# Performance work log

Hardware: AMD Instinct MI355X
Metric: run time of the kernel (lower is better)

## Reference

```python
import jax, jax.numpy as jnp
import numpy as np

N_NODES = 100000
N_EDGES = 1600000
D = 64
N_LAYERS = 3


def setup_inputs() -> dict:
    key = jax.random.key(0)
    k1, k2, k3, k4 = jax.random.split(key, 4)
    x = jax.random.normal(k1, (N_NODES, D), dtype=jnp.float32)
    edge_index = jax.random.randint(k2, (2, N_EDGES), 0, N_NODES, dtype=jnp.int64)
    scale = 1.0 / np.sqrt(D)
    Wl = jax.random.normal(k3, (N_LAYERS, D, D), dtype=jnp.float32) * scale
    Wr = jax.random.normal(k4, (N_LAYERS, D, D), dtype=jnp.float32) * scale
    b = jnp.zeros((N_LAYERS, D), dtype=jnp.float32)
    return {"x": x, "edge_index": edge_index, "Wl": Wl, "Wr": Wr, "b": b}


def _sage_conv(x, src, dst, Wl, Wr, b, n_nodes):
    # mean-aggregate source features onto targets, then two linear maps
    msgs = x[src]                                              # [E, d]
    summed = jax.ops.segment_sum(msgs, dst, num_segments=n_nodes)   # [N, d]
    cnt = jax.ops.segment_sum(jnp.ones(src.shape[0], x.dtype), dst,
                              num_segments=n_nodes)            # [N]
    agg = summed / jnp.maximum(cnt, 1.0)[:, None]
    return agg @ Wl + x @ Wr + b


def reference(x, edge_index, Wl, Wr, b):
    # GraphSAGE forward in eval mode (dropout is identity, p=0.5 only in training)
    src, dst = edge_index[0], edge_index[1]
    n = x.shape[0]
    h = x
    for i in range(N_LAYERS - 1):
        h = _sage_conv(h, src, dst, Wl[i], Wr[i], b[i], n)
        h = jax.nn.relu(h)
    h = _sage_conv(h, src, dst, Wl[-1], Wr[-1], b[-1], n)
    return h
```

## Files before the change

kernel.cpp:

```cpp
#include <hip/hip_runtime.h>
#include <hip/hip_fp16.h>

#define DD 64
#define NPB 32
#define EPC 8192
#define BK_SHIFT 9
#define BNODES 512
#define SCHUNK 1024
#define APAD 136

typedef _Float16 half8 __attribute__((ext_vector_type(8)));
typedef float f32x4 __attribute__((ext_vector_type(4)));

union U8 { uint2 u; __half2 h[2]; };

__global__ __launch_bounds__(256) void prep_kernel(
    const float* __restrict__ x, __half* __restrict__ x16, int n8, int nconvb,
    const int* __restrict__ dst, int e, int nc, int* __restrict__ histT, int nbuck,
    const float* __restrict__ Wl, const float* __restrict__ Wr, __half* __restrict__ Wswz)
{
    __shared__ int h[BNODES];
    int bid = blockIdx.x, tid = threadIdx.x;
    if (bid < nconvb) {
        int i = bid * 256 + tid;
        if (i < n8) {
            const float4* p = reinterpret_cast<const float4*>(x + (size_t)i * 8);
            float4 a = p[0], b = p[1];
            __half2* q = reinterpret_cast<__half2*>(x16 + (size_t)i * 8);
            q[0] = __floats2half2_rn(a.x, a.y);
            q[1] = __floats2half2_rn(a.z, a.w);
            q[2] = __floats2half2_rn(b.x, b.y);
            q[3] = __floats2half2_rn(b.z, b.w);
        }
    } else if (bid < nconvb + nc) {
        int c = bid - nconvb;
        for (int i = tid; i < nbuck; i += 256) h[i] = 0;
        __syncthreads();
        int base = c * EPC;
#pragma unroll
        for (int j = 0; j < EPC / 256; ++j) {
            int i = base + j * 256 + tid;
            if (i < e) atomicAdd(&h[dst[i] >> BK_SHIFT], 1);
        }
        __syncthreads();
        for (int b = tid; b < nbuck; b += 256) histT[b * nc + c] = h[b];
    } else {
        int idx = (bid - nconvb - nc) * 256 + tid;
        int total = 3 * 4 * 4 * 64;
        if (idx < total) {
            int lane = idx & 63;
            int nt   = (idx >> 6) & 3;
            int kt   = (idx >> 8) & 3;
            int L    = idx >> 10;
            int nn    = nt * 16 + (lane & 15);
            int kbase = kt * 32 + 8 * (lane >> 4);
            __half* o = Wswz + (size_t)idx * 8;
#pragma unroll
            for (int i = 0; i < 8; ++i) {
                int k = kbase + i;
                float v = (k < 64) ? Wl[(size_t)L * 4096 + (size_t)k * 64 + nn]
                                   : Wr[(size_t)L * 4096 + (size_t)(k - 64) * 64 + nn];
                o[i] = __float2half(v);
            }
        }
    }
}

__global__ __launch_bounds__(256) void scan_part_kernel(const int* __restrict__ data, int tot,
                                                        int* __restrict__ blocksum) {
    __shared__ int red[256];
    int tid = threadIdx.x;
    int base = blockIdx.x * SCHUNK + tid * 4;
    int s = 0;
#pragma unroll
    for (int j = 0; j < 4; ++j) {
        int i = base + j;
        if (i < tot) s += data[i];
    }
    red[tid] = s;
    __syncthreads();
    for (int off = 128; off > 0; off >>= 1) {
        if (tid < off) red[tid] += red[tid + off];
        __syncthreads();
    }
    if (tid == 0) blocksum[blockIdx.x] = red[0];
}

__global__ __launch_bounds__(256) void scan_write_kernel(int* __restrict__ data, int tot,
                                                         const int* __restrict__ blocksum, int nsb) {
    __shared__ int sc[256];
    __shared__ int soff;
    int tid = threadIdx.x;
    if (tid < 64) {
        int v = (tid < (int)blockIdx.x && tid < nsb) ? blocksum[tid] : 0;
#pragma unroll
        for (int off = 32; off > 0; off >>= 1) v += __shfl_down(v, off);
        if (tid == 0) soff = v;
    }
    int base = blockIdx.x * SCHUNK + tid * 4;
    int e0 = 0, e1 = 0, e2 = 0, e3 = 0;
    if (base + 0 < tot) e0 = data[base + 0];
    if (base + 1 < tot) e1 = data[base + 1];
    if (base + 2 < tot) e2 = data[base + 2];
    if (base + 3 < tot) e3 = data[base + 3];
    int s = e0 + e1 + e2 + e3;
    sc[tid] = s;
    __syncthreads();
    for (int off = 1; off < 256; off <<= 1) {
        int t = (tid >= off) ? sc[tid - off] : 0;
        __syncthreads();
        sc[tid] += t;
        __syncthreads();
    }
    int run = soff + sc[tid] - s;
    if (base + 0 < tot) data[base + 0] = run;
    if (base + 1 < tot) data[base + 1] = run + e0;
    if (base + 2 < tot) data[base + 2] = run + e0 + e1;
    if (base + 3 < tot) data[base + 3] = run + e0 + e1 + e2;
}

__global__ __launch_bounds__(256) void binB_kernel(const int* __restrict__ src, const int* __restrict__ dst,
                                                   int e, int nc, const int* __restrict__ offT,
                                                   int nbuck, int* __restrict__ binned) {
    __shared__ int cur[BNODES];
    int tid = threadIdx.x, c = blockIdx.x;
    for (int b = tid; b < nbuck; b += 256) cur[b] = offT[b * nc + c];
    __syncthreads();
    int base = c * EPC;
#pragma unroll
    for (int j = 0; j < EPC / 256; ++j) {
        int i = base + j * 256 + tid;
        if (i < e) {
            int d = dst[i];
            int p = atomicAdd(&cur[d >> BK_SHIFT], 1);
            binned[p] = (int)(((unsigned)(d & (BNODES - 1)) << 23) | (unsigned)src[i]);
        }
    }
}

__global__ __launch_bounds__(BNODES) void place_kernel(const int* __restrict__ binned,
                                                       const int* __restrict__ offT, int nc,
                                                       int nbuck, int e, int n,
                                                       int* __restrict__ rowp, int* __restrict__ esrc) {
    __shared__ int deg[BNODES];
    __shared__ int sc[BNODES];
    int tid = threadIdx.x, b = blockIdx.x;
    int node0 = b << BK_SHIFT;
    int base = offT[b * nc];
    int end  = (b + 1 < nbuck) ? offT[(b + 1) * nc] : e;
    deg[tid] = 0;
    __syncthreads();
    for (int i = base + tid; i < end; i += BNODES)
        atomicAdd(&deg[(unsigned)binned[i] >> 23], 1);
    __syncthreads();
    int v = deg[tid];
    sc[tid] = v;
    __syncthreads();
    for (int off = 1; off < BNODES; off <<= 1) {
        int t = (tid >= off) ? sc[tid - off] : 0;
        __syncthreads();
        sc[tid] += t;
        __syncthreads();
    }
    int excl = sc[tid] - v;
    int node = node0 + tid;
    if (node < n) rowp[node] = base + excl;
    if (b == 0 && tid == 0) rowp[n] = e;
    deg[tid] = base + excl;
    __syncthreads();
    for (int i = base + tid; i < end; i += BNODES) {
        int p = binned[i];
        int pos = atomicAdd(&deg[(unsigned)p >> 23], 1);
        esrc[pos] = p & 0x7FFFFF;
    }
}

__global__ __launch_bounds__(512) void sage_layer_kernel(
    const __half* __restrict__ hin16,
    const int* __restrict__ rowp, const int* __restrict__ esrc,
    const __half* __restrict__ Bfrag,
    const float* __restrict__ bias,
    float* __restrict__ out32, __half* __restrict__ out16,
    int n, int relu)
{
    __shared__ _Float16 sA[NPB][APAD];

    int tid = threadIdx.x;
    int grp = tid >> 4;
    int l   = tid & 15;
    int node = blockIdx.x * NPB + grp;

    if (node < n) {
        uint2 sv = *reinterpret_cast<const uint2*>(hin16 + (size_t)node * DD + l * 4);
        *reinterpret_cast<uint2*>(&sA[grp][64 + 4 * l]) = sv;

        int beg = rowp[node], end = rowp[node + 1];
        float ax = 0.f, ay = 0.f, az = 0.f, aw = 0.f;
        int t = beg;
        for (; t + 8 <= end; t += 8) {
            int s0 = esrc[t + 0], s1 = esrc[t + 1], s2 = esrc[t + 2], s3 = esrc[t + 3];
            int s4 = esrc[t + 4], s5 = esrc[t + 5], s6 = esrc[t + 6], s7 = esrc[t + 7];
            U8 v0, v1, v2, v3, v4, v5, v6, v7;
            v0.u = *reinterpret_cast<const uint2*>(hin16 + (size_t)s0 * DD + l * 4);
            v1.u = *reinterpret_cast<const uint2*>(hin16 + (size_t)s1 * DD + l * 4);
            v2.u = *reinterpret_cast<const uint2*>(hin16 + (size_t)s2 * DD + l * 4);
            v3.u = *reinterpret_cast<const uint2*>(hin16 + (size_t)s3 * DD + l * 4);
            v4.u = *reinterpret_cast<const uint2*>(hin16 + (size_t)s4 * DD + l * 4);
            v5.u = *reinterpret_cast<const uint2*>(hin16 + (size_t)s5 * DD + l * 4);
            v6.u = *reinterpret_cast<const uint2*>(hin16 + (size_t)s6 * DD + l * 4);
            v7.u = *reinterpret_cast<const uint2*>(hin16 + (size_t)s7 * DD + l * 4);
            float2 a0 = __half22float2(v0.h[0]), b0 = __half22float2(v0.h[1]);
            float2 a1 = __half22float2(v1.h[0]), b1 = __half22float2(v1.h[1]);
            float2 a2 = __half22float2(v2.h[0]), b2 = __half22float2(v2.h[1]);
            float2 a3 = __half22float2(v3.h[0]), b3 = __half22float2(v3.h[1]);
            float2 a4 = __half22float2(v4.h[0]), b4 = __half22float2(v4.h[1]);
            float2 a5 = __half22float2(v5.h[0]), b5 = __half22float2(v5.h[1]);
            float2 a6 = __half22float2(v6.h[0]), b6 = __half22float2(v6.h[1]);
            float2 a7 = __half22float2(v7.h[0]), b7 = __half22float2(v7.h[1]);
            ax += ((a0.x + a1.x) + (a2.x + a3.x)) + ((a4.x + a5.x) + (a6.x + a7.x));
            ay += ((a0.y + a1.y) + (a2.y + a3.y)) + ((a4.y + a5.y) + (a6.y + a7.y));
            az += ((b0.x + b1.x) + (b2.x + b3.x)) + ((b4.x + b5.x) + (b6.x + b7.x));
            aw += ((b0.y + b1.y) + (b2.y + b3.y)) + ((b4.y + b5.y) + (b6.y + b7.y));
        }
        if (t + 4 <= end) {
            int s0 = esrc[t + 0], s1 = esrc[t + 1], s2 = esrc[t + 2], s3 = esrc[t + 3];
            U8 v0, v1, v2, v3;
            v0.u = *reinterpret_cast<const uint2*>(hin16 + (size_t)s0 * DD + l * 4);
            v1.u = *reinterpret_cast<const uint2*>(hin16 + (size_t)s1 * DD + l * 4);
            v2.u = *reinterpret_cast<const uint2*>(hin16 + (size_t)s2 * DD + l * 4);
            v3.u = *reinterpret_cast<const uint2*>(hin16 + (size_t)s3 * DD + l * 4);
            float2 a0 = __half22float2(v0.h[0]), b0 = __half22float2(v0.h[1]);
            float2 a1 = __half22float2(v1.h[0]), b1 = __half22float2(v1.h[1]);
            float2 a2 = __half22float2(v2.h[0]), b2 = __half22float2(v2.h[1]);
            float2 a3 = __half22float2(v3.h[0]), b3 = __half22float2(v3.h[1]);
            ax += (a0.x + a1.x) + (a2.x + a3.x);
            ay += (a0.y + a1.y) + (a2.y + a3.y);
            az += (b0.x + b1.x) + (b2.x + b3.x);
            aw += (b0.y + b1.y) + (b2.y + b3.y);
            t += 4;
        }
        for (; t < end; ++t) {
            int s = esrc[t];
            U8 v; v.u = *reinterpret_cast<const uint2*>(hin16 + (size_t)s * DD + l * 4);
            float2 f0 = __half22float2(v.h[0]), f1 = __half22float2(v.h[1]);
            ax += f0.x; ay += f0.y; az += f1.x; aw += f1.y;
        }
        float inv = 1.0f / fmaxf((float)(end - beg), 1.0f);
        U8 pk; pk.h[0] = __floats2half2_rn(ax * inv, ay * inv);
               pk.h[1] = __floats2half2_rn(az * inv, aw * inv);
        *reinterpret_cast<uint2*>(&sA[grp][4 * l]) = pk.u;
    }
    __syncthreads();

    int wave  = tid >> 6;
    int lane  = tid & 63;
    int mtile = wave >> 2;
    int nt    = wave & 3;
    int arow  = mtile * 16 + (lane & 15);
    f32x4 acc = {0.f, 0.f, 0.f, 0.f};
    const half8* bfr = reinterpret_cast<const half8*>(Bfrag);
#pragma unroll
    for (int kt = 0; kt < 4; ++kt) {
        half8 a = *reinterpret_cast<const half8*>(&sA[arow][kt * 32 + 8 * (lane >> 4)]);
        half8 b = bfr[(kt * 4 + nt) * 64 + lane];
        acc = __builtin_amdgcn_mfma_f32_16x16x32_f16(a, b, acc, 0, 0, 0);
    }
    int col = nt * 16 + (lane & 15);
    float bv = bias[col];
    int rbase = blockIdx.x * NPB + mtile * 16 + (lane >> 4) * 4;
#pragma unroll
    for (int j = 0; j < 4; ++j) {
        int r = rbase + j;
        if (r < n) {
            float o = acc[j] + bv;
            if (relu) o = fmaxf(o, 0.f);
            if (out32) out32[(size_t)r * DD + col] = o;
            if (out16) out16[(size_t)r * DD + col] = __float2half(o);
        }
    }
}

extern "C" void kernel_launch(void* const* d_in, const int* in_sizes, int n_in,
                              void* d_out, int out_size, void* d_ws, size_t ws_size,
                              hipStream_t stream) {
    (void)n_in; (void)out_size; (void)ws_size;
    const float* x  = (const float*)d_in[0];
    const int*   ei = (const int*)d_in[1];
    const float* Wl = (const float*)d_in[2];
    const float* Wr = (const float*)d_in[3];
    const float* bb = (const float*)d_in[4];
    float* out = (float*)d_out;

    int n = in_sizes[0] / DD;
    int e = in_sizes[1] / 2;
    const int* src = ei;
    const int* dst = ei + e;

    int nc    = (e + EPC - 1) / EPC;
    int nbuck = (n + BNODES - 1) >> BK_SHIFT;
    int tot   = nbuck * nc;
    int nsb   = (tot + SCHUNK - 1) / SCHUNK;

    char* cur = (char*)d_ws;
    auto alloc = [&](size_t bytes) -> void* {
        void* p = (void*)cur;
        cur += (bytes + 255) & ~(size_t)255;
        return p;
    };
    int*    histT  = (int*)alloc((size_t)tot * 4);
    int*    bsum   = (int*)alloc(1024 * 4);
    int*    binned = (int*)alloc((size_t)e * 4);
    int*    rowp   = (int*)alloc(((size_t)n + 1) * 4);
    int*    esrc   = (int*)alloc((size_t)e * 4);
    __half* x16    = (__half*)alloc((size_t)n * DD * 2);
    __half* hA16   = (__half*)alloc((size_t)n * DD * 2);
    __half* hB16   = (__half*)alloc((size_t)n * DD * 2);
    __half* Wswz   = (__half*)alloc((size_t)3 * 8192 * 2);

    int n8     = n * DD / 8;
    int nconvb = (n8 + 255) / 256;
    int nwswzb = (3 * 4 * 4 * 64 + 255) / 256;
    prep_kernel<<<nconvb + nc + nwswzb, 256, 0, stream>>>(
        x, x16, n8, nconvb, dst, e, nc, histT, nbuck, Wl, Wr, Wswz);

    scan_part_kernel<<<nsb, 256, 0, stream>>>(histT, tot, bsum);
    scan_write_kernel<<<nsb, 256, 0, stream>>>(histT, tot, bsum, nsb);
    binB_kernel<<<nc, 256, 0, stream>>>(src, dst, e, nc, histT, nbuck, binned);
    place_kernel<<<nbuck, BNODES, 0, stream>>>(binned, histT, nc, nbuck, e, n, rowp, esrc);

    int lb = (n + NPB - 1) / NPB;
    sage_layer_kernel<<<lb, 512, 0, stream>>>(x16,  rowp, esrc, Wswz,         bb,          nullptr, hA16, n, 1);
    sage_layer_kernel<<<lb, 512, 0, stream>>>(hA16, rowp, esrc, Wswz + 8192,  bb + DD,     nullptr, hB16, n, 1);
    sage_layer_kernel<<<lb, 512, 0, stream>>>(hB16, rowp, esrc, Wswz + 16384, bb + 2 * DD, out,     nullptr, n, 0);
}
```

Before: 181.0 us.

## Fold histogram scan into binning and placement kernels, dropping two scan launches

Removes the two separate scan kernels over the bucket-by-chunk histogram. Each binning block and each placement block now rebuilds the offsets it needs: one thread per bucket sums its row (and the prefix up to its chunk), followed by a shared-memory scan across buckets. This saves two kernel launches and their dependency gaps, at the cost of every block redundantly reading the whole histogram (196x196 ints) and running serial row loops of about 196 iterations. It also assumes nbuck is at most 256.

```diff
diff --git a/kernel.cpp b/kernel.cpp
--- a/kernel.cpp
+++ b/kernel.cpp
@@ -6,7 +6,6 @@
 #define EPC 8192
 #define BK_SHIFT 9
 #define BNODES 512
-#define SCHUNK 1024
 #define APAD 136
 
 typedef _Float16 half8 __attribute__((ext_vector_type(8)));
@@ -66,65 +65,32 @@
     }
 }
 
-__global__ __launch_bounds__(256) void scan_part_kernel(const int* __restrict__ data, int tot,
-                                                        int* __restrict__ blocksum) {
-    __shared__ int red[256];
-    int tid = threadIdx.x;
-    int base = blockIdx.x * SCHUNK + tid * 4;
-    int s = 0;
-#pragma unroll
-    for (int j = 0; j < 4; ++j) {
-        int i = base + j;
-        if (i < tot) s += data[i];
-    }
-    red[tid] = s;
-    __syncthreads();
-    for (int off = 128; off > 0; off >>= 1) {
-        if (tid < off) red[tid] += red[tid + off];
-        __syncthreads();
-    }
-    if (tid == 0) blocksum[blockIdx.x] = red[0];
-}
-
-__global__ __launch_bounds__(256) void scan_write_kernel(int* __restrict__ data, int tot,
-                                                         const int* __restrict__ blocksum, int nsb) {
-    __shared__ int sc[256];
-    __shared__ int soff;
-    int tid = threadIdx.x;
-    if (tid < 64) {
-        int v = (tid < (int)blockIdx.x && tid < nsb) ? blocksum[tid] : 0;
-#pragma unroll
-        for (int off = 32; off > 0; off >>= 1) v += __shfl_down(v, off);
-        if (tid == 0) soff = v;
-    }
-    int base = blockIdx.x * SCHUNK + tid * 4;
-    int e0 = 0, e1 = 0, e2 = 0, e3 = 0;
-    if (base + 0 < tot) e0 = data[base + 0];
-    if (base + 1 < tot) e1 = data[base + 1];
-    if (base + 2 < tot) e2 = data[base + 2];
-    if (base + 3 < tot) e3 = data[base + 3];
-    int s = e0 + e1 + e2 + e3;
-    sc[tid] = s;
-    __syncthreads();
-    for (int off = 1; off < 256; off <<= 1) {
-        int t = (tid >= off) ? sc[tid - off] : 0;
-        __syncthreads();
-        sc[tid] += t;
-        __syncthreads();
-    }
-    int run = soff + sc[tid] - s;
-    if (base + 0 < tot) data[base + 0] = run;
-    if (base + 1 < tot) data[base + 1] = run + e0;
-    if (base + 2 < tot) data[base + 2] = run + e0 + e1;
-    if (base + 3 < tot) data[base + 3] = run + e0 + e1 + e2;
-}
-
 __global__ __launch_bounds__(256) void binB_kernel(const int* __restrict__ src, const int* __restrict__ dst,
-                                                   int e, int nc, const int* __restrict__ offT,
+                                                   int e, int nc, const int* __restrict__ histT,
                                                    int nbuck, int* __restrict__ binned) {
+    __shared__ int rsc[256];
     __shared__ int cur[BNODES];
     int tid = threadIdx.x, c = blockIdx.x;
-    for (int b = tid; b < nbuck; b += 256) cur[b] = offT[b * nc + c];
+    int myrow = 0, mypart = 0;
+    if (tid < nbuck) {
+        const int* row = histT + (size_t)tid * nc;
+        int s = 0, p = 0;
+        for (int cc = 0; cc < nc; ++cc) {
+            int v = row[cc];
+            s += v;
+            p += (cc < c) ? v : 0;
+        }
+        myrow = s; mypart = p;
+    }
+    rsc[tid] = myrow;
+    __syncthreads();
+    for (int off = 1; off < 256; off <<= 1) {
+        int t = (tid >= off) ? rsc[tid - off] : 0;
+        __syncthreads();
+        rsc[tid] += t;
+        __syncthreads();
+    }
+    if (tid < nbuck) cur[tid] = (rsc[tid] - myrow) + mypart;
     __syncthreads();
     int base = c * EPC;
 #pragma unroll
@@ -139,15 +105,34 @@
 }
 
 __global__ __launch_bounds__(BNODES) void place_kernel(const int* __restrict__ binned,
-                                                       const int* __restrict__ offT, int nc,
+                                                       const int* __restrict__ histT, int nc,
                                                        int nbuck, int e, int n,
                                                        int* __restrict__ rowp, int* __restrict__ esrc) {
+    __shared__ int rsum[256];
+    __shared__ int rsc[256];
     __shared__ int deg[BNODES];
     __shared__ int sc[BNODES];
     int tid = threadIdx.x, b = blockIdx.x;
+    if (tid < 256) {
+        int s = 0;
+        if (tid < nbuck) {
+            const int* row = histT + (size_t)tid * nc;
+            for (int cc = 0; cc < nc; ++cc) s += row[cc];
+        }
+        rsum[tid] = s;
+        rsc[tid] = s;
+    }
+    __syncthreads();
+    for (int off = 1; off < 256; off <<= 1) {
+        int t = (tid >= off && tid < 256) ? rsc[tid - off] : 0;
+        __syncthreads();
+        if (tid < 256) rsc[tid] += t;
+        __syncthreads();
+    }
+    int base = rsc[b] - rsum[b];
+    int end  = rsc[b];
+
     int node0 = b << BK_SHIFT;
-    int base = offT[b * nc];
-    int end  = (b + 1 < nbuck) ? offT[(b + 1) * nc] : e;
     deg[tid] = 0;
     __syncthreads();
     for (int i = base + tid; i < end; i += BNODES)
@@ -299,7 +284,6 @@
     int nc    = (e + EPC - 1) / EPC;
     int nbuck = (n + BNODES - 1) >> BK_SHIFT;
     int tot   = nbuck * nc;
-    int nsb   = (tot + SCHUNK - 1) / SCHUNK;
 
     char* cur = (char*)d_ws;
     auto alloc = [&](size_t bytes) -> void* {
@@ -308,7 +292,6 @@
         return p;
     };
     int*    histT  = (int*)alloc((size_t)tot * 4);
-    int*    bsum   = (int*)alloc(1024 * 4);
     int*    binned = (int*)alloc((size_t)e * 4);
     int*    rowp   = (int*)alloc(((size_t)n + 1) * 4);
     int*    esrc   = (int*)alloc((size_t)e * 4);
@@ -323,8 +306,6 @@
     prep_kernel<<<nconvb + nc + nwswzb, 256, 0, stream>>>(
         x, x16, n8, nconvb, dst, e, nc, histT, nbuck, Wl, Wr, Wswz);
 
-    scan_part_kernel<<<nsb, 256, 0, stream>>>(histT, tot, bsum);
-    scan_write_kernel<<<nsb, 256, 0, stream>>>(histT, tot, bsum, nsb);
     binB_kernel<<<nc, 256, 0, stream>>>(src, dst, e, nc, histT, nbuck, binned);
     place_kernel<<<nbuck, BNODES, 0, stream>>>(binned, histT, nc, nbuck, e, n, rowp, esrc);
 
```

Measured after the change: 209.0 us. +15.5%, slower.
